# Kernel optimization log

Hardware: AMD Instinct MI355X
Metric: run time of the kernel (lower is better)

## Reference

```python
import jax, jax.numpy as jnp
import numpy as np

DIM = 512
B, QL, KL = 8, 1024, 4096

def setup_inputs() -> dict:
    key = jax.random.key(0)
    k1, k2, k3 = jax.random.split(key, 3)
    output = jax.random.normal(k1, (B, QL, DIM), dtype=jnp.float32)
    context = jax.random.normal(k2, (B, KL, DIM), dtype=jnp.float32)
    # nn.Linear(2*dim, dim): weight [dim, 2*dim]; store transposed [2*dim, dim]
    W_out = jax.random.normal(k3, (DIM, 2 * DIM), dtype=jnp.float32) * (1.0 / np.sqrt(2 * DIM))
    b_out = jnp.zeros((DIM,), dtype=jnp.float32)
    return {"output": output, "context": context, "W_out": W_out, "b_out": b_out}

def reference(output, context, W_out, b_out):
    # scores: [B, QL, KL]
    attn = jnp.einsum("bqd,bkd->bqk", output, context)
    attn = jax.nn.softmax(attn, axis=-1)
    # mix: [B, QL, D]
    mix = jnp.einsum("bqk,bkd->bqd", attn, context)
    combined = jnp.concatenate([mix, output], axis=-1)  # [B, QL, 2D]
    out = jnp.tanh(jnp.einsum("bqe,de->bqd", combined, W_out) + b_out)
    return (out, attn)
```

## Files before the change

### kernel.cpp

```cpp
#include <hip/hip_runtime.h>
#include <math.h>

#define DIMM 512
#define NB 8
#define QLEN 1024
#define KLEN 4096

typedef __attribute__((ext_vector_type(4))) float floatx4;
typedef __attribute__((ext_vector_type(8))) short short8;
typedef __attribute__((ext_vector_type(4))) unsigned short ushort4v;
typedef __attribute__((ext_vector_type(8))) unsigned short ushort8v;

static __device__ __forceinline__ unsigned short f2bf(float f) {
    unsigned u = __builtin_bit_cast(unsigned, f);
    u += 0x7FFFu + ((u >> 16) & 1u);
    return (unsigned short)(u >> 16);
}
static __device__ __forceinline__ float bf2f(unsigned short h) {
    unsigned u = ((unsigned)h) << 16;
    return __builtin_bit_cast(float, u);
}

static __device__ __forceinline__ void gload16(const unsigned short* g, unsigned short* l) {
    __builtin_amdgcn_global_load_lds(
        (__attribute__((address_space(1))) void*)const_cast<unsigned short*>(g),
        (__attribute__((address_space(3))) void*)l,
        16, 0, 0);
}

__global__ __launch_bounds__(256) void split_k(const float* __restrict__ x,
                                               unsigned short* __restrict__ dst) {
    int idx = blockIdx.x * 256 + threadIdx.x;
    float4 v = ((const float4*)x)[idx];
    int r = idx >> 7;
    int c = (idx & 127) << 2;
    float f[4] = {v.x, v.y, v.z, v.w};
    ushort4v hi, lo;
#pragma unroll
    for (int e = 0; e < 4; ++e) {
        unsigned short h = f2bf(f[e]);
        hi[e] = h;
        lo[e] = f2bf(f[e] - bf2f(h));
    }
    unsigned short* row = dst + ((size_t)r << 10);
    *(ushort4v*)(row + c) = hi;
    *(ushort4v*)(row + 512 + c) = lo;
}

__global__ __launch_bounds__(256) void conv_hi(const float* __restrict__ x,
                                               unsigned short* __restrict__ dst,
                                               int c4shift, int ldd, int off) {
    int idx = blockIdx.x * 256 + threadIdx.x;
    float4 v = ((const float4*)x)[idx];
    int r = idx >> c4shift;
    int c = (idx & ((1 << c4shift) - 1)) << 2;
    ushort4v hi;
    hi[0] = f2bf(v.x); hi[1] = f2bf(v.y); hi[2] = f2bf(v.z); hi[3] = f2bf(v.w);
    *(ushort4v*)(dst + (size_t)r * ldd + off + c) = hi;
}

__global__ __launch_bounds__(256) void trans_hi(const float* __restrict__ ctx,
                                                unsigned short* __restrict__ ctxT) {
    __shared__ unsigned short tile[64][66];
    int b = blockIdx.z;
    int c0 = blockIdx.x * 64;
    int k0 = blockIdx.y * 64;
    const float* src = ctx + ((size_t)b * KLEN + k0) * DIMM + c0;
    int t = threadIdx.x;
    int rr = t >> 4, cc4 = (t & 15) * 4;
#pragma unroll
    for (int it = 0; it < 4; ++it) {
        int r = rr + it * 16;
        float4 v = *(const float4*)(src + (size_t)r * DIMM + cc4);
        tile[r][cc4 + 0] = f2bf(v.x);
        tile[r][cc4 + 1] = f2bf(v.y);
        tile[r][cc4 + 2] = f2bf(v.z);
        tile[r][cc4 + 3] = f2bf(v.w);
    }
    __syncthreads();
#pragma unroll
    for (int it = 0; it < 2; ++it) {
        int u = t + it * 256;
        int c = u >> 3;
        int kk = (u & 7) * 8;
        ushort8v o;
#pragma unroll
        for (int e = 0; e < 8; ++e) o[e] = tile[kk + e][c];
        *(ushort8v*)(ctxT + ((size_t)b * DIMM + c0 + c) * KLEN + k0 + kk) = o;
    }
}

__global__ __launch_bounds__(256) void softmax_k(float* __restrict__ S,
                                                 unsigned short* __restrict__ Pb) {
    size_t row = blockIdx.x;
    float* p = S + row * KLEN;
    int t = threadIdx.x;
    int lane = t & 63, wv = t >> 6;
    float4 v[4];
    float mx = -3.0e38f;
#pragma unroll
    for (int i = 0; i < 4; ++i) {
        v[i] = *(const float4*)(p + i * 1024 + t * 4);
        mx = fmaxf(mx, fmaxf(fmaxf(v[i].x, v[i].y), fmaxf(v[i].z, v[i].w)));
    }
#pragma unroll
    for (int m = 32; m >= 1; m >>= 1) mx = fmaxf(mx, __shfl_xor(mx, m, 64));
    __shared__ float redm[4], reds[4];
    if (lane == 0) redm[wv] = mx;
    __syncthreads();
    mx = fmaxf(fmaxf(redm[0], redm[1]), fmaxf(redm[2], redm[3]));
    float sum = 0.f;
#pragma unroll
    for (int i = 0; i < 4; ++i) {
        v[i].x = __expf(v[i].x - mx); v[i].y = __expf(v[i].y - mx);
        v[i].z = __expf(v[i].z - mx); v[i].w = __expf(v[i].w - mx);
        sum += v[i].x + v[i].y + v[i].z + v[i].w;
    }
#pragma unroll
    for (int m = 32; m >= 1; m >>= 1) sum += __shfl_xor(sum, m, 64);
    if (lane == 0) reds[wv] = sum;
    __syncthreads();
    float inv = 1.0f / (reds[0] + reds[1] + reds[2] + reds[3]);
    unsigned short* pb = Pb + row * KLEN;
#pragma unroll
    for (int i = 0; i < 4; ++i) {
        float4 w;
        w.x = v[i].x * inv; w.y = v[i].y * inv; w.z = v[i].z * inv; w.w = v[i].w * inv;
        *(float4*)(p + i * 1024 + t * 4) = w;
        ushort4v h;
        h[0] = f2bf(w.x); h[1] = f2bf(w.y); h[2] = f2bf(w.z); h[3] = f2bf(w.w);
        *(ushort4v*)(pb + i * 1024 + t * 4) = h;
    }
}

template <int EPI, bool REMAP, int BN>
__global__ __launch_bounds__(256) void gemm_bt(
    const unsigned short* __restrict__ A,
    const unsigned short* __restrict__ Bm,
    float* __restrict__ Cf, unsigned short* __restrict__ Cb,
    const float* __restrict__ bias,
    int Ktiles, long lda, long ldb, long ldc,
    long a_bs, long b_bs, long c_bs) {
    constexpr int NF = BN / 32;
    __shared__ unsigned short sA[128 * 64];
    __shared__ unsigned short sB[BN * 64];
    const int tid = threadIdx.x;
    const int lane = tid & 63;
    const int wv = tid >> 6;
    const int wm = wv >> 1, wn = wv & 1;
    const int mlane = lane & 15, quad = lane >> 4;
    const unsigned short* Ab = A + (size_t)blockIdx.z * a_bs + (size_t)blockIdx.y * 128 * lda;
    const unsigned short* Bb = Bm + (size_t)blockIdx.z * b_bs + (size_t)blockIdx.x * BN * ldb;
    const int r8 = tid >> 3;
    const int c8 = (tid & 7) << 3;
    const int cg = ((tid & 7) ^ ((tid >> 3) & 7)) << 3;
    unsigned short* la = sA + r8 * 64 + c8;
    unsigned short* lb = sB + r8 * 64 + c8;

    floatx4 acc[4][NF] = {};

    for (int kt = 0; kt < Ktiles; ++kt) {
        long kv = (long)kt * 64;
        long ka = REMAP ? (kv >= 512 ? kv - 512 : kv) : kv;
        long kb = REMAP ? (kv >= 1024 ? kv - 1024 : kv) : kv;
        if (kt) __syncthreads();
        const unsigned short* ga = Ab + (size_t)r8 * lda + ka + cg;
        const unsigned short* gb = Bb + (size_t)r8 * ldb + kb + cg;
#pragma unroll
        for (int it = 0; it < 4; ++it)
            gload16(ga + (size_t)(it * 32) * lda, la + it * 2048);
#pragma unroll
        for (int it = 0; it < BN / 32; ++it)
            gload16(gb + (size_t)(it * 32) * ldb, lb + it * 2048);
        __syncthreads();
#pragma unroll
        for (int s = 0; s < 2; ++s) {
            const int swz = (((s * 4 + quad) ^ (mlane & 7)) << 3);
            short8 af[4], bf[NF];
#pragma unroll
            for (int i = 0; i < 4; ++i)
                af[i] = *(const short8*)(sA + (wm * 64 + i * 16 + mlane) * 64 + swz);
#pragma unroll
            for (int j = 0; j < NF; ++j)
                bf[j] = *(const short8*)(sB + (wn * (BN / 2) + j * 16 + mlane) * 64 + swz);
#pragma unroll
            for (int i = 0; i < 4; ++i)
#pragma unroll
                for (int j = 0; j < NF; ++j)
                    acc[i][j] = __builtin_amdgcn_mfma_f32_16x16x32_bf16(af[i], bf[j], acc[i][j], 0, 0, 0);
        }
    }

    size_t crow0 = (size_t)blockIdx.y * 128 + wm * 64 + quad * 4;
    size_t ccol0 = (size_t)blockIdx.x * BN + wn * (BN / 2) + mlane;
    size_t cbase = (size_t)blockIdx.z * c_bs;
#pragma unroll
    for (int i = 0; i < 4; ++i) {
#pragma unroll
        for (int j = 0; j < NF; ++j) {
            size_t gr = crow0 + i * 16;
            size_t gc = ccol0 + j * 16;
#pragma unroll
            for (int r = 0; r < 4; ++r) {
                float vv = acc[i][j][r];
                size_t off = cbase + (gr + r) * ldc + gc;
                if (EPI == 0) Cf[off] = vv;
                else if (EPI == 1) Cb[off] = f2bf(vv);
                else Cf[off] = tanhf(vv + bias[gc]);
            }
        }
    }
}

extern "C" void kernel_launch(void* const* d_in, const int* in_sizes, int n_in,
                              void* d_out, int out_size, void* d_ws, size_t ws_size,
                              hipStream_t stream) {
    (void)in_sizes; (void)n_in; (void)out_size; (void)ws_size;
    const float* outp = (const float*)d_in[0];
    const float* ctx  = (const float*)d_in[1];
    const float* W    = (const float*)d_in[2];
    const float* bias = (const float*)d_in[3];

    float* out0 = (float*)d_out;
    float* attn = out0 + (size_t)NB * QLEN * DIMM;

    unsigned char* w = (unsigned char*)d_ws;
    unsigned short* R1 = (unsigned short*)(w);
    unsigned short* R2 = (unsigned short*)(w + (16ull << 20));
    unsigned short* R3 = (unsigned short*)(w + (80ull << 20));
    unsigned short* R4 = (unsigned short*)(w + (112ull << 20));

    split_k<<<4096, 256, 0, stream>>>(outp, R1);
    split_k<<<16384, 256, 0, stream>>>(ctx, R2);
    trans_hi<<<dim3(8, 64, 8), 256, 0, stream>>>(ctx, R3);
    conv_hi<<<512, 256, 0, stream>>>(W, R4, 8, 1024, 0);

    gemm_bt<0, true, 128><<<dim3(32, 8, 8), 256, 0, stream>>>(
        R1, R2, attn, nullptr, nullptr,
        24, 1024, 1024, 4096,
        (long)QLEN * 1024, (long)KLEN * 1024, (long)QLEN * KLEN);

    softmax_k<<<8192, 256, 0, stream>>>(attn, R2);

    conv_hi<<<4096, 256, 0, stream>>>(outp, R1, 7, 1024, 512);

    gemm_bt<1, false, 64><<<dim3(8, 8, 8), 256, 0, stream>>>(
        R2, R3, nullptr, R1, nullptr,
        64, 4096, 4096, 1024,
        (long)QLEN * KLEN, (long)DIMM * KLEN, (long)QLEN * 1024);

    gemm_bt<2, false, 64><<<dim3(8, 64, 1), 256, 0, stream>>>(
        R1, R4, out0, nullptr, bias,
        16, 1024, 1024, 512, 0, 0, 0);
}
```

Measured before the change: 505.5 us.

## Switch GEMMs to 32x32x16 MFMA, fuse context prep, use fast tanh

The GEMM kernel now uses 32x32x16 bf16 MFMA instructions with 2xNJ accumulator tiles in place of 16x16x32 tiles. Each wave reads fewer LDS fragments per MFMA, and the epilogue indexing is remapped to match. The split hi/lo conversion of the context is fused into the transpose kernel, so the context is read once instead of twice. The launch bounds also request 4 waves per SIMD, and tanh is replaced with an exp-based approximation, which may change register allocation and add small numerical error.

```diff
diff --git a/kernel.cpp b/kernel.cpp
--- a/kernel.cpp
+++ b/kernel.cpp
@@ -6,7 +6,7 @@
 #define QLEN 1024
 #define KLEN 4096
 
-typedef __attribute__((ext_vector_type(4))) float floatx4;
+typedef __attribute__((ext_vector_type(16))) float floatx16;
 typedef __attribute__((ext_vector_type(8))) short short8;
 typedef __attribute__((ext_vector_type(4))) unsigned short ushort4v;
 typedef __attribute__((ext_vector_type(8))) unsigned short ushort8v;
@@ -19,6 +19,11 @@
 static __device__ __forceinline__ float bf2f(unsigned short h) {
     unsigned u = ((unsigned)h) << 16;
     return __builtin_bit_cast(float, u);
+}
+static __device__ __forceinline__ float fast_tanh(float x) {
+    float e = __expf(-2.0f * fabsf(x));
+    float t = (1.0f - e) / (1.0f + e);
+    return copysignf(t, x);
 }
 
 static __device__ __forceinline__ void gload16(const unsigned short* g, unsigned short* l) {
@@ -59,23 +64,32 @@
     *(ushort4v*)(dst + (size_t)r * ldd + off + c) = hi;
 }
 
-__global__ __launch_bounds__(256) void trans_hi(const float* __restrict__ ctx,
+__global__ __launch_bounds__(256) void prep_ctx(const float* __restrict__ ctx,
+                                                unsigned short* __restrict__ hilo,
                                                 unsigned short* __restrict__ ctxT) {
     __shared__ unsigned short tile[64][66];
     int b = blockIdx.z;
     int c0 = blockIdx.x * 64;
     int k0 = blockIdx.y * 64;
     const float* src = ctx + ((size_t)b * KLEN + k0) * DIMM + c0;
+    unsigned short* hl = hilo + ((size_t)b * KLEN + k0) * 1024 + c0;
     int t = threadIdx.x;
     int rr = t >> 4, cc4 = (t & 15) * 4;
 #pragma unroll
     for (int it = 0; it < 4; ++it) {
         int r = rr + it * 16;
         float4 v = *(const float4*)(src + (size_t)r * DIMM + cc4);
-        tile[r][cc4 + 0] = f2bf(v.x);
-        tile[r][cc4 + 1] = f2bf(v.y);
-        tile[r][cc4 + 2] = f2bf(v.z);
-        tile[r][cc4 + 3] = f2bf(v.w);
+        float f[4] = {v.x, v.y, v.z, v.w};
+        ushort4v hi, lo;
+#pragma unroll
+        for (int e = 0; e < 4; ++e) {
+            unsigned short h = f2bf(f[e]);
+            hi[e] = h;
+            lo[e] = f2bf(f[e] - bf2f(h));
+            tile[r][cc4 + e] = h;
+        }
+        *(ushort4v*)(hl + (size_t)r * 1024 + cc4) = hi;
+        *(ushort4v*)(hl + (size_t)r * 1024 + 512 + cc4) = lo;
     }
     __syncthreads();
 #pragma unroll
@@ -134,21 +148,21 @@
 }
 
 template <int EPI, bool REMAP, int BN>
-__global__ __launch_bounds__(256) void gemm_bt(
+__global__ __launch_bounds__(256, 4) void gemm_bt(
     const unsigned short* __restrict__ A,
     const unsigned short* __restrict__ Bm,
     float* __restrict__ Cf, unsigned short* __restrict__ Cb,
     const float* __restrict__ bias,
     int Ktiles, long lda, long ldb, long ldc,
     long a_bs, long b_bs, long c_bs) {
-    constexpr int NF = BN / 32;
+    constexpr int NJ = BN / 64;
     __shared__ unsigned short sA[128 * 64];
     __shared__ unsigned short sB[BN * 64];
     const int tid = threadIdx.x;
     const int lane = tid & 63;
     const int wv = tid >> 6;
     const int wm = wv >> 1, wn = wv & 1;
-    const int mlane = lane & 15, quad = lane >> 4;
+    const int m32 = lane & 31, half = lane >> 5;
     const unsigned short* Ab = A + (size_t)blockIdx.z * a_bs + (size_t)blockIdx.y * 128 * lda;
     const unsigned short* Bb = Bm + (size_t)blockIdx.z * b_bs + (size_t)blockIdx.x * BN * ldb;
     const int r8 = tid >> 3;
@@ -157,7 +171,7 @@
     unsigned short* la = sA + r8 * 64 + c8;
     unsigned short* lb = sB + r8 * 64 + c8;
 
-    floatx4 acc[4][NF] = {};
+    floatx16 acc[2][NJ] = {};
 
     for (int kt = 0; kt < Ktiles; ++kt) {
         long kv = (long)kt * 64;
@@ -174,39 +188,42 @@
             gload16(gb + (size_t)(it * 32) * ldb, lb + it * 2048);
         __syncthreads();
 #pragma unroll
-        for (int s = 0; s < 2; ++s) {
-            const int swz = (((s * 4 + quad) ^ (mlane & 7)) << 3);
-            short8 af[4], bf[NF];
-#pragma unroll
-            for (int i = 0; i < 4; ++i)
-                af[i] = *(const short8*)(sA + (wm * 64 + i * 16 + mlane) * 64 + swz);
-#pragma unroll
-            for (int j = 0; j < NF; ++j)
-                bf[j] = *(const short8*)(sB + (wn * (BN / 2) + j * 16 + mlane) * 64 + swz);
-#pragma unroll
-            for (int i = 0; i < 4; ++i)
-#pragma unroll
-                for (int j = 0; j < NF; ++j)
-                    acc[i][j] = __builtin_amdgcn_mfma_f32_16x16x32_bf16(af[i], bf[j], acc[i][j], 0, 0, 0);
+        for (int s = 0; s < 4; ++s) {
+            const int swz = (((s * 2 + half) ^ (lane & 7)) << 3);
+            short8 af[2], bf[NJ];
+#pragma unroll
+            for (int i = 0; i < 2; ++i)
+                af[i] = *(const short8*)(sA + (wm * 64 + i * 32 + m32) * 64 + swz);
+#pragma unroll
+            for (int j = 0; j < NJ; ++j)
+                bf[j] = *(const short8*)(sB + (wn * (BN / 2) + j * 32 + m32) * 64 + swz);
+#pragma unroll
+            for (int i = 0; i < 2; ++i)
+#pragma unroll
+                for (int j = 0; j < NJ; ++j)
+                    acc[i][j] = __builtin_amdgcn_mfma_f32_32x32x16_bf16(af[i], bf[j], acc[i][j], 0, 0, 0);
         }
     }
 
-    size_t crow0 = (size_t)blockIdx.y * 128 + wm * 64 + quad * 4;
-    size_t ccol0 = (size_t)blockIdx.x * BN + wn * (BN / 2) + mlane;
+    size_t crow0 = (size_t)blockIdx.y * 128 + wm * 64 + half * 4;
+    size_t ccol0 = (size_t)blockIdx.x * BN + wn * (BN / 2) + m32;
     size_t cbase = (size_t)blockIdx.z * c_bs;
 #pragma unroll
-    for (int i = 0; i < 4; ++i) {
-#pragma unroll
-        for (int j = 0; j < NF; ++j) {
-            size_t gr = crow0 + i * 16;
-            size_t gc = ccol0 + j * 16;
-#pragma unroll
-            for (int r = 0; r < 4; ++r) {
-                float vv = acc[i][j][r];
-                size_t off = cbase + (gr + r) * ldc + gc;
-                if (EPI == 0) Cf[off] = vv;
-                else if (EPI == 1) Cb[off] = f2bf(vv);
-                else Cf[off] = tanhf(vv + bias[gc]);
+    for (int i = 0; i < 2; ++i) {
+#pragma unroll
+        for (int j = 0; j < NJ; ++j) {
+            size_t gc = ccol0 + j * 32;
+#pragma unroll
+            for (int r2 = 0; r2 < 4; ++r2) {
+#pragma unroll
+                for (int r1 = 0; r1 < 4; ++r1) {
+                    float vv = acc[i][j][r2 * 4 + r1];
+                    size_t gr = crow0 + i * 32 + r2 * 8 + r1;
+                    size_t off = cbase + gr * ldc + gc;
+                    if (EPI == 0) Cf[off] = vv;
+                    else if (EPI == 1) Cb[off] = f2bf(vv);
+                    else Cf[off] = fast_tanh(vv + bias[gc]);
+                }
             }
         }
     }
@@ -231,8 +248,7 @@
     unsigned short* R4 = (unsigned short*)(w + (112ull << 20));
 
     split_k<<<4096, 256, 0, stream>>>(outp, R1);
-    split_k<<<16384, 256, 0, stream>>>(ctx, R2);
-    trans_hi<<<dim3(8, 64, 8), 256, 0, stream>>>(ctx, R3);
+    prep_ctx<<<dim3(8, 64, 8), 256, 0, stream>>>(ctx, R2, R3);
     conv_hi<<<512, 256, 0, stream>>>(W, R4, 8, 1024, 0);
 
     gemm_bt<0, true, 128><<<dim3(32, 8, 8), 256, 0, stream>>>(
```

Result: no change. 501.7 us (-0.7%).

## Fuse context hi/lo split into transpose kernel and reuse split output buffer

Applied to the files above, without the earlier changes.

Merges the context hi/lo bf16 split into the transpose kernel so context is read once, and swaps the hi/lo halves of the split output so its hi part already sits where the final GEMM expects the concatenated output. This removes the separate conv_hi pass, with the first GEMM's k-remap adjusted to match. It also adds an occupancy hint to launch bounds, interleaves B-fragment loads with the MFMAs to cut register pressure, and replaces tanhf with an exp-based approximation. The fast tanh and the remap change carry small accuracy and correctness risk.

```diff
diff --git a/kernel.cpp b/kernel.cpp
--- a/kernel.cpp
+++ b/kernel.cpp
@@ -19,6 +19,11 @@
 static __device__ __forceinline__ float bf2f(unsigned short h) {
     unsigned u = ((unsigned)h) << 16;
     return __builtin_bit_cast(float, u);
+}
+static __device__ __forceinline__ float fast_tanh(float x) {
+    float e = __expf(-2.0f * fabsf(x));
+    float t = (1.0f - e) / (1.0f + e);
+    return copysignf(t, x);
 }
 
 static __device__ __forceinline__ void gload16(const unsigned short* g, unsigned short* l) {
@@ -43,8 +48,8 @@
         lo[e] = f2bf(f[e] - bf2f(h));
     }
     unsigned short* row = dst + ((size_t)r << 10);
-    *(ushort4v*)(row + c) = hi;
-    *(ushort4v*)(row + 512 + c) = lo;
+    *(ushort4v*)(row + c) = lo;
+    *(ushort4v*)(row + 512 + c) = hi;
 }
 
 __global__ __launch_bounds__(256) void conv_hi(const float* __restrict__ x,
@@ -59,23 +64,32 @@
     *(ushort4v*)(dst + (size_t)r * ldd + off + c) = hi;
 }
 
-__global__ __launch_bounds__(256) void trans_hi(const float* __restrict__ ctx,
+__global__ __launch_bounds__(256) void prep_ctx(const float* __restrict__ ctx,
+                                                unsigned short* __restrict__ hilo,
                                                 unsigned short* __restrict__ ctxT) {
     __shared__ unsigned short tile[64][66];
     int b = blockIdx.z;
     int c0 = blockIdx.x * 64;
     int k0 = blockIdx.y * 64;
     const float* src = ctx + ((size_t)b * KLEN + k0) * DIMM + c0;
+    unsigned short* hl = hilo + ((size_t)b * KLEN + k0) * 1024 + c0;
     int t = threadIdx.x;
     int rr = t >> 4, cc4 = (t & 15) * 4;
 #pragma unroll
     for (int it = 0; it < 4; ++it) {
         int r = rr + it * 16;
         float4 v = *(const float4*)(src + (size_t)r * DIMM + cc4);
-        tile[r][cc4 + 0] = f2bf(v.x);
-        tile[r][cc4 + 1] = f2bf(v.y);
-        tile[r][cc4 + 2] = f2bf(v.z);
-        tile[r][cc4 + 3] = f2bf(v.w);
+        float f[4] = {v.x, v.y, v.z, v.w};
+        ushort4v hi, lo;
+#pragma unroll
+        for (int e = 0; e < 4; ++e) {
+            unsigned short h = f2bf(f[e]);
+            hi[e] = h;
+            lo[e] = f2bf(f[e] - bf2f(h));
+            tile[r][cc4 + e] = h;
+        }
+        *(ushort4v*)(hl + (size_t)r * 1024 + cc4) = hi;
+        *(ushort4v*)(hl + (size_t)r * 1024 + 512 + cc4) = lo;
     }
     __syncthreads();
 #pragma unroll
@@ -134,7 +148,7 @@
 }
 
 template <int EPI, bool REMAP, int BN>
-__global__ __launch_bounds__(256) void gemm_bt(
+__global__ __launch_bounds__(256, 4) void gemm_bt(
     const unsigned short* __restrict__ A,
     const unsigned short* __restrict__ Bm,
     float* __restrict__ Cf, unsigned short* __restrict__ Cb,
@@ -161,8 +175,11 @@
 
     for (int kt = 0; kt < Ktiles; ++kt) {
         long kv = (long)kt * 64;
-        long ka = REMAP ? (kv >= 512 ? kv - 512 : kv) : kv;
-        long kb = REMAP ? (kv >= 1024 ? kv - 1024 : kv) : kv;
+        long ka = kv, kb = kv;
+        if (REMAP) {
+            ka = kv < 512 ? kv + 512 : (kv < 1024 ? kv : kv - 1024);
+            kb = kv < 1024 ? kv : kv - 1024;
+        }
         if (kt) __syncthreads();
         const unsigned short* ga = Ab + (size_t)r8 * lda + ka + cg;
         const unsigned short* gb = Bb + (size_t)r8 * ldb + kb + cg;
@@ -176,18 +193,17 @@
 #pragma unroll
         for (int s = 0; s < 2; ++s) {
             const int swz = (((s * 4 + quad) ^ (mlane & 7)) << 3);
-            short8 af[4], bf[NF];
+            short8 af[4];
 #pragma unroll
             for (int i = 0; i < 4; ++i)
                 af[i] = *(const short8*)(sA + (wm * 64 + i * 16 + mlane) * 64 + swz);
 #pragma unroll
-            for (int j = 0; j < NF; ++j)
-                bf[j] = *(const short8*)(sB + (wn * (BN / 2) + j * 16 + mlane) * 64 + swz);
-#pragma unroll
-            for (int i = 0; i < 4; ++i)
-#pragma unroll
-                for (int j = 0; j < NF; ++j)
-                    acc[i][j] = __builtin_amdgcn_mfma_f32_16x16x32_bf16(af[i], bf[j], acc[i][j], 0, 0, 0);
+            for (int j = 0; j < NF; ++j) {
+                short8 bfj = *(const short8*)(sB + (wn * (BN / 2) + j * 16 + mlane) * 64 + swz);
+#pragma unroll
+                for (int i = 0; i < 4; ++i)
+                    acc[i][j] = __builtin_amdgcn_mfma_f32_16x16x32_bf16(af[i], bfj, acc[i][j], 0, 0, 0);
+            }
         }
     }
 
@@ -206,7 +222,7 @@
                 size_t off = cbase + (gr + r) * ldc + gc;
                 if (EPI == 0) Cf[off] = vv;
                 else if (EPI == 1) Cb[off] = f2bf(vv);
-                else Cf[off] = tanhf(vv + bias[gc]);
+                else Cf[off] = fast_tanh(vv + bias[gc]);
             }
         }
     }
@@ -231,8 +247,7 @@
     unsigned short* R4 = (unsigned short*)(w + (112ull << 20));
 
     split_k<<<4096, 256, 0, stream>>>(outp, R1);
-    split_k<<<16384, 256, 0, stream>>>(ctx, R2);
-    trans_hi<<<dim3(8, 64, 8), 256, 0, stream>>>(ctx, R3);
+    prep_ctx<<<dim3(8, 64, 8), 256, 0, stream>>>(ctx, R2, R3);
     conv_hi<<<512, 256, 0, stream>>>(W, R4, 8, 1024, 0);
 
     gemm_bt<0, true, 128><<<dim3(32, 8, 8), 256, 0, stream>>>(
@@ -242,8 +257,6 @@
 
     softmax_k<<<8192, 256, 0, stream>>>(attn, R2);
 
-    conv_hi<<<4096, 256, 0, stream>>>(outp, R1, 7, 1024, 512);
-
     gemm_bt<1, false, 64><<<dim3(8, 8, 8), 256, 0, stream>>>(
         R2, R3, nullptr, R1, nullptr,
         64, 4096, 4096, 1024,
```

Result: faster. 477.0 us (-5.6%).
